# Performance work log

Measured on AMD Instinct MI355X. Metric: run time of the kernel, lower is better.

## Reference

```python
import jax, jax.numpy as jnp
import numpy as np

N = 100000   # nodes
E = 1200000  # edges
D = 64       # in_channels == out_channels, heads=1
NEG_SLOPE = 0.2  # PyG GATv2Conv default negative_slope


def setup_inputs() -> dict:
    key = jax.random.key(0)
    k1, k2, k3, k4 = jax.random.split(key, 4)
    x = jax.random.normal(k1, (N, D), dtype=jnp.float32)
    edge_index = jax.random.randint(k2, (2, E), 0, N, dtype=jnp.int32)
    # glorot-ish scale for shared linear (share_weights=True -> lin_l == lin_r)
    W = jax.random.normal(k3, (D, D), dtype=jnp.float32) * (1.0 / np.sqrt(D))
    b = jnp.zeros((D,), dtype=jnp.float32)
    att = jax.random.normal(k4, (D,), dtype=jnp.float32) * (1.0 / np.sqrt(D))
    return {"x": x, "edge_index": edge_index, "W": W, "b": b, "att": att}


def reference(x, edge_index, W, b, att):
    src = edge_index[0]  # source j (messages flow j -> i)
    dst = edge_index[1]  # target i
    # shared linear transform (share_weights=True)
    z = x @ W.T + b                                   # [N, D]
    # GATv2 score: att . leakyrelu(z_j + z_i)
    e = jax.nn.leaky_relu(z[src] + z[dst], NEG_SLOPE) @ att  # [E]
    # segment softmax over incoming edges of each target node
    m = jax.ops.segment_max(e, dst, num_segments=N)   # [N]
    ex = jnp.exp(e - m[dst])                          # [E]
    s = jax.ops.segment_sum(ex, dst, num_segments=N)  # [N]
    alpha = ex / s[dst]                               # [E]
    # SimpleConv(aggr='sum') with edge_weight=alpha on ORIGINAL x
    out = jax.ops.segment_sum(alpha[:, None] * x[src], dst, num_segments=N)  # [N, D]
    return out
```

## Files before the change

kernel.cpp:

```cpp
#include <hip/hip_runtime.h>

#define D 64
#define LOG2E 1.4426950408889634f

#define HEPT_H 32
#define SEPT 32
#define BSH 7
#define BSZ 128

using frag_ab = __attribute__((ext_vector_type(8))) short;
using f32x4   = __attribute__((ext_vector_type(4))) float;

__device__ __forceinline__ unsigned short f2bf(float f) {
    unsigned int bits = __float_as_uint(f);
    return (unsigned short)((bits + 0x7fffu + ((bits >> 16) & 1u)) >> 16);
}

__device__ __forceinline__ frag_ab pack8(float4 a, float4 b) {
    frag_ab f;
    f[0] = (short)f2bf(a.x); f[1] = (short)f2bf(a.y);
    f[2] = (short)f2bf(a.z); f[3] = (short)f2bf(a.w);
    f[4] = (short)f2bf(b.x); f[5] = (short)f2bf(b.y);
    f[6] = (short)f2bf(b.z); f[7] = (short)f2bf(b.w);
    return f;
}

__global__ __launch_bounds__(256) void gemm_z_hist(const float* __restrict__ x,
                                                   const float* __restrict__ W,
                                                   const float* __restrict__ b,
                                                   unsigned int* __restrict__ zxb,
                                                   int n,
                                                   const int* __restrict__ dst,
                                                   int* __restrict__ hist2d,
                                                   int e_cnt, int histBlk,
                                                   int nb, int nblk) {
    __shared__ int cnt[2048];
    int tid = threadIdx.x;

    if ((int)blockIdx.x < histBlk) {
        for (int i = tid; i < nb; i += 256) cnt[i] = 0;
        __syncthreads();
        int base = blockIdx.x * (256 * HEPT_H);
        for (int j = 0; j < HEPT_H; ++j) {
            int e = base + j * 256 + tid;
            if (e < e_cnt) atomicAdd(&cnt[dst[e] >> BSH], 1);
        }
        __syncthreads();
        for (int i = tid; i < nb; i += 256)
            hist2d[(size_t)i * nblk + blockIdx.x] = cnt[i];
        return;
    }

    int row0 = (blockIdx.x - histBlk) * 64;
    int l  = tid & 63;
    int w  = tid >> 6;
    int lr = l & 15;
    int hi = l >> 4;
    int lk = hi * 8;

    int arow = row0 + w * 16 + lr;
    int crow = (arow < n) ? arow : (n - 1);
    const float* xp = x + (size_t)crow * 64;
    frag_ab afr[2];
#pragma unroll
    for (int ks = 0; ks < 2; ++ks) {
        const float* ap = xp + ks * 32 + lk;
        afr[ks] = pack8(*(const float4*)ap, *(const float4*)(ap + 4));
    }

    frag_ab bfr[4][2];
#pragma unroll
    for (int colt = 0; colt < 4; ++colt) {
#pragma unroll
        for (int ks = 0; ks < 2; ++ks) {
            const float* wp = W + (colt * 16 + lr) * 64 + ks * 32 + lk;
            bfr[colt][ks] = pack8(*(const float4*)wp, *(const float4*)(wp + 4));
        }
    }

    f32x4 zero = {0.f, 0.f, 0.f, 0.f};
    f32x4 acc[4] = {zero, zero, zero, zero};
#pragma unroll
    for (int ks = 0; ks < 2; ++ks) {
#pragma unroll
        for (int colt = 0; colt < 4; ++colt) {
            acc[colt] = __builtin_amdgcn_mfma_f32_16x16x32_bf16(
                afr[ks], bfr[colt][ks], acc[colt], 0, 0, 0);
        }
    }

#pragma unroll
    for (int colt = 0; colt < 4; ++colt) {
        int col = colt * 16 + lr;
        float bb = b[col];
#pragma unroll
        for (int r = 0; r < 4; ++r) {
            int row = row0 + w * 16 + hi * 4 + r;
            int rrow = (row < n) ? row : (n - 1);
            float z  = acc[colt][r] + bb;
            float xv = x[(size_t)rrow * 64 + col];
            unsigned int u = (unsigned int)f2bf(z) |
                             ((unsigned int)f2bf(xv) << 16);
            if (row < n)
                zxb[(size_t)row * 64 + col] = u;
        }
    }
}

__global__ __launch_bounds__(256) void scan_part(const int* __restrict__ data,
                                                 int* __restrict__ part, int n) {
    __shared__ int red[256];
    int t = threadIdx.x;
    int i = blockIdx.x * 256 + t;
    red[t] = (i < n) ? data[i] : 0;
    __syncthreads();
    for (int off = 128; off >= 1; off >>= 1) {
        if (t < off) red[t] += red[t + off];
        __syncthreads();
    }
    if (t == 0) part[blockIdx.x] = red[0];
}

__global__ __launch_bounds__(1024) void scan_top(int* __restrict__ part, int B) {
    __shared__ int s[1024];
    int t = threadIdx.x;
    int v = (t < B) ? part[t] : 0;
    s[t] = v;
    __syncthreads();
    for (int off = 1; off < 1024; off <<= 1) {
        int u = (t >= off) ? s[t - off] : 0;
        __syncthreads();
        s[t] += u;
        __syncthreads();
    }
    if (t < B) part[t] = s[t] - v;
}

__global__ __launch_bounds__(256) void scan_final_ip(int* data,
                                                     const int* __restrict__ part, int n) {
    __shared__ int s[256];
    int t = threadIdx.x;
    int i = blockIdx.x * 256 + t;
    int v = (i < n) ? data[i] : 0;
    s[t] = v;
    __syncthreads();
    for (int off = 1; off < 256; off <<= 1) {
        int u = (t >= off) ? s[t - off] : 0;
        __syncthreads();
        s[t] += u;
        __syncthreads();
    }
    int incl = s[t] + part[blockIdx.x];
    if (i < n) data[i] = incl - v;
    if (i == n - 1) data[n] = incl;
}

__global__ __launch_bounds__(256) void msd_scatter(const int* __restrict__ src,
                                                   const int* __restrict__ dst,
                                                   const int* __restrict__ histS,
                                                   unsigned int* __restrict__ packed,
                                                   int e_cnt, int nb, int nblk) {
    __shared__ int cnt[1024];
    int t = threadIdx.x;
    int blk = blockIdx.x;
    for (int i = t; i < nb; i += 256) cnt[i] = histS[(size_t)i * nblk + blk];
    __syncthreads();
    int base = blk * (256 * SEPT);
    for (int j = 0; j < SEPT; ++j) {
        int e = base + j * 256 + t;
        if (e < e_cnt) {
            int d = dst[e];
            int pos = atomicAdd(&cnt[d >> BSH], 1);
            packed[pos] = (unsigned int)src[e] | ((unsigned int)(d & (BSZ - 1)) << 24);
        }
    }
}

__global__ __launch_bounds__(256) void bucket_csr(const unsigned int* __restrict__ packed,
                                                  const int* __restrict__ histS,
                                                  int* __restrict__ rowstart,
                                                  int* __restrict__ srcids,
                                                  int n, int e_cnt, int nb, int nblk) {
    __shared__ int cnt[128];
    __shared__ int sc[128];
    __shared__ int cur[128];
    int t = threadIdx.x;
    int b = blockIdx.x;
    int lo = histS[(size_t)b * nblk];
    int hi = histS[(size_t)(b + 1) * nblk];
    int m = hi - lo;

    if (t < 128) cnt[t] = 0;
    __syncthreads();
    for (int i = t; i < m; i += 256)
        atomicAdd(&cnt[packed[lo + i] >> 24], 1);
    __syncthreads();
    if (t < 128) sc[t] = cnt[t];
    __syncthreads();
    for (int off = 1; off < 128; off <<= 1) {
        int u = (t < 128 && t >= off) ? sc[t - off] : 0;
        __syncthreads();
        if (t < 128) sc[t] += u;
        __syncthreads();
    }
    if (t < 128) {
        int excl = sc[t] - cnt[t];
        cur[t] = lo + excl;
        int node = (b << BSH) + t;
        if (node < n) rowstart[node] = lo + excl;
    }
    if (b == nb - 1 && t == 0) rowstart[n] = e_cnt;
    __syncthreads();
    for (int i = t; i < m; i += 256) {
        unsigned int p = packed[lo + i];
        int pos = atomicAdd(&cur[p >> 24], 1);
        srcids[pos] = (int)(p & 0xFFFFFFu);
    }
}

__global__ __launch_bounds__(256) void gather4b(const int* __restrict__ srcids,
                                                const int* __restrict__ rowstart,
                                                const unsigned int* __restrict__ zxb,
                                                const float* __restrict__ att,
                                                float* __restrict__ out, int n) {
    int lane = threadIdx.x & 63;
    int node = blockIdx.x * 4 + (threadIdx.x >> 6);
    if (node >= n) return;
    int q = lane & 15;
    int h = lane >> 4;
    int rs = rowstart[node], re = rowstart[node + 1];

    const uint4 zdv = *(const uint4*)(zxb + (size_t)node * 64 + 4 * q);
    float zd0 = __uint_as_float(zdv.x << 16);
    float zd1 = __uint_as_float(zdv.y << 16);
    float zd2 = __uint_as_float(zdv.z << 16);
    float zd3 = __uint_as_float(zdv.w << 16);
    float4 av = *(const float4*)(att + 4 * q);
    float a0 = av.x * LOG2E, a1 = av.y * LOG2E, a2 = av.z * LOG2E, a3 = av.w * LOG2E;

    float ax0 = 0.f, ax1 = 0.f, ax2 = 0.f, ax3 = 0.f, ssum = 0.f;
    int efull = rs + ((re - rs) & ~7);
    int e = rs;
    for (; e < efull; e += 8) {
        int s0 = srcids[e + h];
        int s1 = srcids[e + 4 + h];
        const uint4 r0 = *(const uint4*)(zxb + (size_t)s0 * 64 + 4 * q);
        const uint4 r1 = *(const uint4*)(zxb + (size_t)s1 * 64 + 4 * q);

        float v0 = __uint_as_float(r0.x << 16) + zd0; v0 = fmaxf(v0, 0.2f * v0);
        float v1 = __uint_as_float(r0.y << 16) + zd1; v1 = fmaxf(v1, 0.2f * v1);
        float v2 = __uint_as_float(r0.z << 16) + zd2; v2 = fmaxf(v2, 0.2f * v2);
        float v3 = __uint_as_float(r0.w << 16) + zd3; v3 = fmaxf(v3, 0.2f * v3);
        float p0 = v0 * a0 + v1 * a1 + v2 * a2 + v3 * a3;

        float u0 = __uint_as_float(r1.x << 16) + zd0; u0 = fmaxf(u0, 0.2f * u0);
        float u1 = __uint_as_float(r1.y << 16) + zd1; u1 = fmaxf(u1, 0.2f * u1);
        float u2 = __uint_as_float(r1.z << 16) + zd2; u2 = fmaxf(u2, 0.2f * u2);
        float u3 = __uint_as_float(r1.w << 16) + zd3; u3 = fmaxf(u3, 0.2f * u3);
        float p1 = u0 * a0 + u1 * a1 + u2 * a2 + u3 * a3;

#pragma unroll
        for (int off = 8; off >= 1; off >>= 1) {
            p0 += __shfl_xor(p0, off, 64);
            p1 += __shfl_xor(p1, off, 64);
        }
        float ex0 = __builtin_exp2f(p0);
        float ex1 = __builtin_exp2f(p1);
        ssum += ex0 + ex1;
        ax0 += ex0 * __uint_as_float(r0.x & 0xffff0000u)
             + ex1 * __uint_as_float(r1.x & 0xffff0000u);
        ax1 += ex0 * __uint_as_float(r0.y & 0xffff0000u)
             + ex1 * __uint_as_float(r1.y & 0xffff0000u);
        ax2 += ex0 * __uint_as_float(r0.z & 0xffff0000u)
             + ex1 * __uint_as_float(r1.z & 0xffff0000u);
        ax3 += ex0 * __uint_as_float(r0.w & 0xffff0000u)
             + ex1 * __uint_as_float(r1.w & 0xffff0000u);
    }
    if (e < re) {
        int e0i = e + h, e1i = e + 4 + h;
        bool l0 = e0i < re, l1 = e1i < re;
        int s0 = l0 ? srcids[e0i] : node;
        int s1 = l1 ? srcids[e1i] : node;
        const uint4 r0 = *(const uint4*)(zxb + (size_t)s0 * 64 + 4 * q);
        const uint4 r1 = *(const uint4*)(zxb + (size_t)s1 * 64 + 4 * q);

        float v0 = __uint_as_float(r0.x << 16) + zd0; v0 = fmaxf(v0, 0.2f * v0);
        float v1 = __uint_as_float(r0.y << 16) + zd1; v1 = fmaxf(v1, 0.2f * v1);
        float v2 = __uint_as_float(r0.z << 16) + zd2; v2 = fmaxf(v2, 0.2f * v2);
        float v3 = __uint_as_float(r0.w << 16) + zd3; v3 = fmaxf(v3, 0.2f * v3);
        float p0 = v0 * a0 + v1 * a1 + v2 * a2 + v3 * a3;

        float u0 = __uint_as_float(r1.x << 16) + zd0; u0 = fmaxf(u0, 0.2f * u0);
        float u1 = __uint_as_float(r1.y << 16) + zd1; u1 = fmaxf(u1, 0.2f * u1);
        float u2 = __uint_as_float(r1.z << 16) + zd2; u2 = fmaxf(u2, 0.2f * u2);
        float u3 = __uint_as_float(r1.w << 16) + zd3; u3 = fmaxf(u3, 0.2f * u3);
        float p1 = u0 * a0 + u1 * a1 + u2 * a2 + u3 * a3;

#pragma unroll
        for (int off = 8; off >= 1; off >>= 1) {
            p0 += __shfl_xor(p0, off, 64);
            p1 += __shfl_xor(p1, off, 64);
        }
        float ex0 = l0 ? __builtin_exp2f(p0) : 0.f;
        float ex1 = l1 ? __builtin_exp2f(p1) : 0.f;
        ssum += ex0 + ex1;
        ax0 += ex0 * __uint_as_float(r0.x & 0xffff0000u)
             + ex1 * __uint_as_float(r1.x & 0xffff0000u);
        ax1 += ex0 * __uint_as_float(r0.y & 0xffff0000u)
             + ex1 * __uint_as_float(r1.y & 0xffff0000u);
        ax2 += ex0 * __uint_as_float(r0.z & 0xffff0000u)
             + ex1 * __uint_as_float(r1.z & 0xffff0000u);
        ax3 += ex0 * __uint_as_float(r0.w & 0xffff0000u)
             + ex1 * __uint_as_float(r1.w & 0xffff0000u);
    }
    ssum += __shfl_xor(ssum, 16, 64); ssum += __shfl_xor(ssum, 32, 64);
    ax0  += __shfl_xor(ax0, 16, 64);  ax0  += __shfl_xor(ax0, 32, 64);
    ax1  += __shfl_xor(ax1, 16, 64);  ax1  += __shfl_xor(ax1, 32, 64);
    ax2  += __shfl_xor(ax2, 16, 64);  ax2  += __shfl_xor(ax2, 32, 64);
    ax3  += __shfl_xor(ax3, 16, 64);  ax3  += __shfl_xor(ax3, 32, 64);
    if (h == 0) {
        float inv = (re > rs) ? 1.f / ssum : 0.f;
        float4 o = make_float4(ax0 * inv, ax1 * inv, ax2 * inv, ax3 * inv);
        *(float4*)&out[(size_t)node * D + 4 * q] = o;
    }
}

extern "C" void kernel_launch(void* const* d_in, const int* in_sizes, int n_in,
                              void* d_out, int out_size, void* d_ws, size_t ws_size,
                              hipStream_t stream) {
    const float* x   = (const float*)d_in[0];
    const int*   ei  = (const int*)d_in[1];
    const float* W   = (const float*)d_in[2];
    const float* b   = (const float*)d_in[3];
    const float* att = (const float*)d_in[4];
    int n = in_sizes[0] / D;
    int e = in_sizes[1] / 2;
    const int* src = ei;
    const int* dst = ei + e;
    float* out = (float*)d_out;

    int gemmBlk = (n + 63) / 64;
    int nb      = (n + BSZ - 1) >> BSH;
    int histBlk = (e + 256 * HEPT_H - 1) / (256 * HEPT_H);
    int nblk    = histBlk;
    int scatBlk = (e + 256 * SEPT - 1) / (256 * SEPT);
    int NBH     = nb * nblk;
    int scanBlk = (NBH + 255) / 256;

    unsigned int* zxb = (unsigned int*)d_ws;
    int* hist2d   = (int*)(zxb + (size_t)n * 64);
    int* rowstart = hist2d + NBH + 1;
    int* srcids   = rowstart + n + 1;
    unsigned int* packed = (unsigned int*)(srcids + e);
    int* part     = (int*)(packed + e);

    gemm_z_hist<<<histBlk + gemmBlk, 256, 0, stream>>>(x, W, b, zxb, n,
                                                       dst, hist2d, e, histBlk, nb, nblk);
    scan_part<<<scanBlk, 256, 0, stream>>>(hist2d, part, NBH);
    scan_top<<<1, 1024, 0, stream>>>(part, scanBlk);
    scan_final_ip<<<scanBlk, 256, 0, stream>>>(hist2d, part, NBH);
    msd_scatter<<<scatBlk, 256, 0, stream>>>(src, dst, hist2d, packed, e, nb, nblk);
    bucket_csr<<<nb, 256, 0, stream>>>(packed, hist2d, rowstart, srcids, n, e, nb, nblk);
    gather4b<<<(n + 3) / 4, 256, 0, stream>>>(srcids, rowstart, zxb, att, out, n);
}
```

Baseline: 194.1 us.

## Fuse CSR construction into a single cooperative kernel with grid syncs

Replaces the histogram, three-pass scan, scatter and bucket-CSR kernels with one cooperative kernel that uses grid.sync between phases, with one block per destination bucket (782 blocks). The histogram is split out of the GEMM kernel into its own stage. The aim is to remove several kernel launches and the inter-kernel gaps. In exchange, all blocks must be co-resident, each block processes more edges (~1535) with less parallelism, and the GEMM no longer overlaps with the histogram.

Result: slower. 561.2 us (+189.1%).

```diff
diff --git a/kernel.cpp b/kernel.cpp
--- a/kernel.cpp
+++ b/kernel.cpp
@@ -1,10 +1,11 @@
 #include <hip/hip_runtime.h>
+#include <hip/hip_cooperative_groups.h>
+
+namespace cg = cooperative_groups;
 
 #define D 64
 #define LOG2E 1.4426950408889634f
 
-#define HEPT_H 32
-#define SEPT 32
 #define BSH 7
 #define BSZ 128
 
@@ -25,33 +26,13 @@
     return f;
 }
 
-__global__ __launch_bounds__(256) void gemm_z_hist(const float* __restrict__ x,
-                                                   const float* __restrict__ W,
-                                                   const float* __restrict__ b,
-                                                   unsigned int* __restrict__ zxb,
-                                                   int n,
-                                                   const int* __restrict__ dst,
-                                                   int* __restrict__ hist2d,
-                                                   int e_cnt, int histBlk,
-                                                   int nb, int nblk) {
-    __shared__ int cnt[2048];
+__global__ __launch_bounds__(256) void gemm_z(const float* __restrict__ x,
+                                              const float* __restrict__ W,
+                                              const float* __restrict__ b,
+                                              unsigned int* __restrict__ zxb,
+                                              int n) {
     int tid = threadIdx.x;
-
-    if ((int)blockIdx.x < histBlk) {
-        for (int i = tid; i < nb; i += 256) cnt[i] = 0;
-        __syncthreads();
-        int base = blockIdx.x * (256 * HEPT_H);
-        for (int j = 0; j < HEPT_H; ++j) {
-            int e = base + j * 256 + tid;
-            if (e < e_cnt) atomicAdd(&cnt[dst[e] >> BSH], 1);
-        }
-        __syncthreads();
-        for (int i = tid; i < nb; i += 256)
-            hist2d[(size_t)i * nblk + blockIdx.x] = cnt[i];
-        return;
-    }
-
-    int row0 = (blockIdx.x - histBlk) * 64;
+    int row0 = blockIdx.x * 64;
     int l  = tid & 63;
     int w  = tid >> 6;
     int lr = l & 15;
@@ -107,114 +88,124 @@
     }
 }
 
-__global__ __launch_bounds__(256) void scan_part(const int* __restrict__ data,
-                                                 int* __restrict__ part, int n) {
+__global__ __launch_bounds__(256) void build_csr(const int* __restrict__ src,
+                                                 const int* __restrict__ dst,
+                                                 int* __restrict__ hist2d,
+                                                 int* __restrict__ rowTot,
+                                                 int* __restrict__ rowBase,
+                                                 int* __restrict__ rowstart,
+                                                 int* __restrict__ srcids,
+                                                 unsigned int* __restrict__ packed,
+                                                 int n, int e_cnt, int nb, int G,
+                                                 int EPB) {
+    cg::grid_group grid = cg::this_grid();
+    __shared__ int cnt[1024];
     __shared__ int red[256];
-    int t = threadIdx.x;
-    int i = blockIdx.x * 256 + t;
-    red[t] = (i < n) ? data[i] : 0;
-    __syncthreads();
-    for (int off = 128; off >= 1; off >>= 1) {
-        if (t < off) red[t] += red[t + off];
-        __syncthreads();
-    }
-    if (t == 0) part[blockIdx.x] = red[0];
-}
-
-__global__ __launch_bounds__(1024) void scan_top(int* __restrict__ part, int B) {
-    __shared__ int s[1024];
-    int t = threadIdx.x;
-    int v = (t < B) ? part[t] : 0;
-    s[t] = v;
-    __syncthreads();
-    for (int off = 1; off < 1024; off <<= 1) {
-        int u = (t >= off) ? s[t - off] : 0;
-        __syncthreads();
-        s[t] += u;
-        __syncthreads();
-    }
-    if (t < B) part[t] = s[t] - v;
-}
-
-__global__ __launch_bounds__(256) void scan_final_ip(int* data,
-                                                     const int* __restrict__ part, int n) {
-    __shared__ int s[256];
-    int t = threadIdx.x;
-    int i = blockIdx.x * 256 + t;
-    int v = (i < n) ? data[i] : 0;
-    s[t] = v;
-    __syncthreads();
-    for (int off = 1; off < 256; off <<= 1) {
-        int u = (t >= off) ? s[t - off] : 0;
-        __syncthreads();
-        s[t] += u;
-        __syncthreads();
-    }
-    int incl = s[t] + part[blockIdx.x];
-    if (i < n) data[i] = incl - v;
-    if (i == n - 1) data[n] = incl;
-}
-
-__global__ __launch_bounds__(256) void msd_scatter(const int* __restrict__ src,
-                                                   const int* __restrict__ dst,
-                                                   const int* __restrict__ histS,
-                                                   unsigned int* __restrict__ packed,
-                                                   int e_cnt, int nb, int nblk) {
-    __shared__ int cnt[1024];
-    int t = threadIdx.x;
-    int blk = blockIdx.x;
-    for (int i = t; i < nb; i += 256) cnt[i] = histS[(size_t)i * nblk + blk];
-    __syncthreads();
-    int base = blk * (256 * SEPT);
-    for (int j = 0; j < SEPT; ++j) {
-        int e = base + j * 256 + t;
-        if (e < e_cnt) {
-            int d = dst[e];
-            int pos = atomicAdd(&cnt[d >> BSH], 1);
-            packed[pos] = (unsigned int)src[e] | ((unsigned int)(d & (BSZ - 1)) << 24);
-        }
-    }
-}
-
-__global__ __launch_bounds__(256) void bucket_csr(const unsigned int* __restrict__ packed,
-                                                  const int* __restrict__ histS,
-                                                  int* __restrict__ rowstart,
-                                                  int* __restrict__ srcids,
-                                                  int n, int e_cnt, int nb, int nblk) {
-    __shared__ int cnt[128];
-    __shared__ int sc[128];
     __shared__ int cur[128];
     int t = threadIdx.x;
     int b = blockIdx.x;
-    int lo = histS[(size_t)b * nblk];
-    int hi = histS[(size_t)(b + 1) * nblk];
-    int m = hi - lo;
-
-    if (t < 128) cnt[t] = 0;
+    int elo = b * EPB;
+    int ehi = elo + EPB; if (ehi > e_cnt) ehi = e_cnt;
+
+    for (int i = t; i < nb; i += 256) cnt[i] = 0;
     __syncthreads();
-    for (int i = t; i < m; i += 256)
-        atomicAdd(&cnt[packed[lo + i] >> 24], 1);
+    for (int e = elo + t; e < ehi; e += 256)
+        atomicAdd(&cnt[dst[e] >> BSH], 1);
     __syncthreads();
-    if (t < 128) sc[t] = cnt[t];
+    for (int i = t; i < nb; i += 256)
+        hist2d[(size_t)i * G + b] = cnt[i];
+    grid.sync();
+
+    {
+        int base = b * G;
+        int j0 = 4 * t;
+        int v0 = (j0 + 0 < G) ? hist2d[base + j0 + 0] : 0;
+        int v1 = (j0 + 1 < G) ? hist2d[base + j0 + 1] : 0;
+        int v2 = (j0 + 2 < G) ? hist2d[base + j0 + 2] : 0;
+        int v3 = (j0 + 3 < G) ? hist2d[base + j0 + 3] : 0;
+        int tsum = v0 + v1 + v2 + v3;
+        red[t] = tsum;
+        __syncthreads();
+        for (int off = 1; off < 256; off <<= 1) {
+            int u = (t >= off) ? red[t - off] : 0;
+            __syncthreads();
+            red[t] += u;
+            __syncthreads();
+        }
+        int excl = red[t] - tsum;
+        if (j0 + 0 < G) hist2d[base + j0 + 0] = excl;
+        if (j0 + 1 < G) hist2d[base + j0 + 1] = excl + v0;
+        if (j0 + 2 < G) hist2d[base + j0 + 2] = excl + v0 + v1;
+        if (j0 + 3 < G) hist2d[base + j0 + 3] = excl + v0 + v1 + v2;
+        if (t == 255) rowTot[b] = red[255];
+    }
+    grid.sync();
+
+    if (b == 0) {
+        int j0 = 4 * t;
+        int v0 = (j0 + 0 < nb) ? rowTot[j0 + 0] : 0;
+        int v1 = (j0 + 1 < nb) ? rowTot[j0 + 1] : 0;
+        int v2 = (j0 + 2 < nb) ? rowTot[j0 + 2] : 0;
+        int v3 = (j0 + 3 < nb) ? rowTot[j0 + 3] : 0;
+        int tsum = v0 + v1 + v2 + v3;
+        red[t] = tsum;
+        __syncthreads();
+        for (int off = 1; off < 256; off <<= 1) {
+            int u = (t >= off) ? red[t - off] : 0;
+            __syncthreads();
+            red[t] += u;
+            __syncthreads();
+        }
+        int excl = red[t] - tsum;
+        if (j0 + 0 < nb) rowBase[j0 + 0] = excl;
+        if (j0 + 1 < nb) rowBase[j0 + 1] = excl + v0;
+        if (j0 + 2 < nb) rowBase[j0 + 2] = excl + v0 + v1;
+        if (j0 + 3 < nb) rowBase[j0 + 3] = excl + v0 + v1 + v2;
+        if (t == 255) rowBase[nb] = red[255];
+    }
+    grid.sync();
+
+    for (int i = t; i < nb; i += 256)
+        cnt[i] = rowBase[i] + hist2d[(size_t)i * G + b];
     __syncthreads();
-    for (int off = 1; off < 128; off <<= 1) {
-        int u = (t < 128 && t >= off) ? sc[t - off] : 0;
-        __syncthreads();
-        if (t < 128) sc[t] += u;
-        __syncthreads();
-    }
-    if (t < 128) {
-        int excl = sc[t] - cnt[t];
-        cur[t] = lo + excl;
-        int node = (b << BSH) + t;
-        if (node < n) rowstart[node] = lo + excl;
-    }
-    if (b == nb - 1 && t == 0) rowstart[n] = e_cnt;
-    __syncthreads();
-    for (int i = t; i < m; i += 256) {
-        unsigned int p = packed[lo + i];
-        int pos = atomicAdd(&cur[p >> 24], 1);
-        srcids[pos] = (int)(p & 0xFFFFFFu);
+    for (int e = elo + t; e < ehi; e += 256) {
+        int d = dst[e];
+        int pos = atomicAdd(&cnt[d >> BSH], 1);
+        packed[pos] = (unsigned int)src[e] | ((unsigned int)(d & (BSZ - 1)) << 24);
+    }
+    grid.sync();
+
+    {
+        int lo = rowBase[b];
+        int hi = rowBase[b + 1];
+        int m = hi - lo;
+        if (t < 128) cnt[t] = 0;
+        __syncthreads();
+        for (int i = t; i < m; i += 256)
+            atomicAdd(&cnt[packed[lo + i] >> 24], 1);
+        __syncthreads();
+        int c = (t < 128) ? cnt[t] : 0;
+        red[t] = c;
+        __syncthreads();
+        for (int off = 1; off < 128; off <<= 1) {
+            int u = (t < 128 && t >= off) ? red[t - off] : 0;
+            __syncthreads();
+            if (t < 128) red[t] += u;
+            __syncthreads();
+        }
+        if (t < 128) {
+            int excl = red[t] - c;
+            cur[t] = lo + excl;
+            int node = (b << BSH) + t;
+            if (node < n) rowstart[node] = lo + excl;
+        }
+        if (b == nb - 1 && t == 0) rowstart[n] = e_cnt;
+        __syncthreads();
+        for (int i = t; i < m; i += 256) {
+            unsigned int p = packed[lo + i];
+            int pos = atomicAdd(&cur[p >> 24], 1);
+            srcids[pos] = (int)(p & 0xFFFFFFu);
+        }
     }
 }
 
@@ -341,25 +332,25 @@
 
     int gemmBlk = (n + 63) / 64;
     int nb      = (n + BSZ - 1) >> BSH;
-    int histBlk = (e + 256 * HEPT_H - 1) / (256 * HEPT_H);
-    int nblk    = histBlk;
-    int scatBlk = (e + 256 * SEPT - 1) / (256 * SEPT);
-    int NBH     = nb * nblk;
-    int scanBlk = (NBH + 255) / 256;
+    int G       = nb;
+    int EPB     = (e + G - 1) / G;
 
     unsigned int* zxb = (unsigned int*)d_ws;
     int* hist2d   = (int*)(zxb + (size_t)n * 64);
-    int* rowstart = hist2d + NBH + 1;
+    int* rowTot   = hist2d + (size_t)nb * G;
+    int* rowBase  = rowTot + nb;
+    int* rowstart = rowBase + nb + 1;
     int* srcids   = rowstart + n + 1;
     unsigned int* packed = (unsigned int*)(srcids + e);
-    int* part     = (int*)(packed + e);
-
-    gemm_z_hist<<<histBlk + gemmBlk, 256, 0, stream>>>(x, W, b, zxb, n,
-                                                       dst, hist2d, e, histBlk, nb, nblk);
-    scan_part<<<scanBlk, 256, 0, stream>>>(hist2d, part, NBH);
-    scan_top<<<1, 1024, 0, stream>>>(part, scanBlk);
-    scan_final_ip<<<scanBlk, 256, 0, stream>>>(hist2d, part, NBH);
-    msd_scatter<<<scatBlk, 256, 0, stream>>>(src, dst, hist2d, packed, e, nb, nblk);
-    bucket_csr<<<nb, 256, 0, stream>>>(packed, hist2d, rowstart, srcids, n, e, nb, nblk);
+
+    gemm_z<<<gemmBlk, 256, 0, stream>>>(x, W, b, zxb, n);
+
+    void* args[] = { (void*)&src, (void*)&dst, (void*)&hist2d, (void*)&rowTot,
+                     (void*)&rowBase, (void*)&rowstart, (void*)&srcids,
+                     (void*)&packed, (void*)&n, (void*)&e, (void*)&nb,
+                     (void*)&G, (void*)&EPB };
+    hipLaunchCooperativeKernel((const void*)build_csr, dim3(G), dim3(256),
+                               args, 0, stream);
+
     gather4b<<<(n + 3) / 4, 256, 0, stream>>>(srcids, rowstart, zxb, att, out, n);
 }
```

## Widen counting-sort buckets to 512 nodes and fuse three-pass scan into one kernel

Applied to the files above, without the earlier changes.

Bucket size for the two-level counting sort grows from 128 to 512 nodes, which cuts the bucket count from about 782 to 196 and shrinks the 2D histogram fourfold. The packed word now stores a 17-bit source id and a 9-bit local destination. With the smaller histogram, the three scan kernels are replaced by one 1024-thread block that scans serial per-thread chunks, removing two launches. bucket_csr uses 512 threads per larger bucket, so there is more shared-atomic contention per block and fewer blocks overall. The 17-bit source field only holds ids below 131072, so correctness now depends on N staying under that limit.

New measurement: 235.6 us. 1.21x slower.

```diff
diff --git a/kernel.cpp b/kernel.cpp
--- a/kernel.cpp
+++ b/kernel.cpp
@@ -5,8 +5,8 @@
 
 #define HEPT_H 32
 #define SEPT 32
-#define BSH 7
-#define BSZ 128
+#define BSH 9
+#define BSZ 512
 
 using frag_ab = __attribute__((ext_vector_type(8))) short;
 using f32x4   = __attribute__((ext_vector_type(4))) float;
@@ -34,7 +34,7 @@
                                                    int* __restrict__ hist2d,
                                                    int e_cnt, int histBlk,
                                                    int nb, int nblk) {
-    __shared__ int cnt[2048];
+    __shared__ int cnt[512];
     int tid = threadIdx.x;
 
     if ((int)blockIdx.x < histBlk) {
@@ -107,52 +107,33 @@
     }
 }
 
-__global__ __launch_bounds__(256) void scan_part(const int* __restrict__ data,
-                                                 int* __restrict__ part, int n) {
-    __shared__ int red[256];
+__global__ __launch_bounds__(1024) void scan_all(int* data, int total_n, int C) {
+    __shared__ int tot[1024];
     int t = threadIdx.x;
-    int i = blockIdx.x * 256 + t;
-    red[t] = (i < n) ? data[i] : 0;
-    __syncthreads();
-    for (int off = 128; off >= 1; off >>= 1) {
-        if (t < off) red[t] += red[t + off];
-        __syncthreads();
-    }
-    if (t == 0) part[blockIdx.x] = red[0];
-}
-
-__global__ __launch_bounds__(1024) void scan_top(int* __restrict__ part, int B) {
-    __shared__ int s[1024];
-    int t = threadIdx.x;
-    int v = (t < B) ? part[t] : 0;
-    s[t] = v;
+    int base = t * C;
+    int s = 0;
+    for (int j = 0; j < C; ++j) {
+        int idx = base + j;
+        if (idx < total_n) s += data[idx];
+    }
+    tot[t] = s;
     __syncthreads();
     for (int off = 1; off < 1024; off <<= 1) {
-        int u = (t >= off) ? s[t - off] : 0;
-        __syncthreads();
-        s[t] += u;
-        __syncthreads();
-    }
-    if (t < B) part[t] = s[t] - v;
-}
-
-__global__ __launch_bounds__(256) void scan_final_ip(int* data,
-                                                     const int* __restrict__ part, int n) {
-    __shared__ int s[256];
-    int t = threadIdx.x;
-    int i = blockIdx.x * 256 + t;
-    int v = (i < n) ? data[i] : 0;
-    s[t] = v;
-    __syncthreads();
-    for (int off = 1; off < 256; off <<= 1) {
-        int u = (t >= off) ? s[t - off] : 0;
-        __syncthreads();
-        s[t] += u;
-        __syncthreads();
-    }
-    int incl = s[t] + part[blockIdx.x];
-    if (i < n) data[i] = incl - v;
-    if (i == n - 1) data[n] = incl;
+        int u = (t >= off) ? tot[t - off] : 0;
+        __syncthreads();
+        tot[t] += u;
+        __syncthreads();
+    }
+    int run = tot[t] - s;
+    for (int j = 0; j < C; ++j) {
+        int idx = base + j;
+        if (idx < total_n) {
+            int v = data[idx];
+            data[idx] = run;
+            run += v;
+        }
+    }
+    if (t == 1023) data[total_n] = tot[1023];
 }
 
 __global__ __launch_bounds__(256) void msd_scatter(const int* __restrict__ src,
@@ -160,7 +141,7 @@
                                                    const int* __restrict__ histS,
                                                    unsigned int* __restrict__ packed,
                                                    int e_cnt, int nb, int nblk) {
-    __shared__ int cnt[1024];
+    __shared__ int cnt[512];
     int t = threadIdx.x;
     int blk = blockIdx.x;
     for (int i = t; i < nb; i += 256) cnt[i] = histS[(size_t)i * nblk + blk];
@@ -171,50 +152,50 @@
         if (e < e_cnt) {
             int d = dst[e];
             int pos = atomicAdd(&cnt[d >> BSH], 1);
-            packed[pos] = (unsigned int)src[e] | ((unsigned int)(d & (BSZ - 1)) << 24);
-        }
-    }
-}
-
-__global__ __launch_bounds__(256) void bucket_csr(const unsigned int* __restrict__ packed,
+            packed[pos] = (unsigned int)src[e] |
+                          ((unsigned int)(d & (BSZ - 1)) << 17);
+        }
+    }
+}
+
+__global__ __launch_bounds__(512) void bucket_csr(const unsigned int* __restrict__ packed,
                                                   const int* __restrict__ histS,
                                                   int* __restrict__ rowstart,
                                                   int* __restrict__ srcids,
                                                   int n, int e_cnt, int nb, int nblk) {
-    __shared__ int cnt[128];
-    __shared__ int sc[128];
-    __shared__ int cur[128];
+    __shared__ int cnt[512];
+    __shared__ int red[512];
+    __shared__ int cur[512];
     int t = threadIdx.x;
     int b = blockIdx.x;
     int lo = histS[(size_t)b * nblk];
     int hi = histS[(size_t)(b + 1) * nblk];
     int m = hi - lo;
 
-    if (t < 128) cnt[t] = 0;
-    __syncthreads();
-    for (int i = t; i < m; i += 256)
-        atomicAdd(&cnt[packed[lo + i] >> 24], 1);
-    __syncthreads();
-    if (t < 128) sc[t] = cnt[t];
-    __syncthreads();
-    for (int off = 1; off < 128; off <<= 1) {
-        int u = (t < 128 && t >= off) ? sc[t - off] : 0;
-        __syncthreads();
-        if (t < 128) sc[t] += u;
-        __syncthreads();
-    }
-    if (t < 128) {
-        int excl = sc[t] - cnt[t];
-        cur[t] = lo + excl;
-        int node = (b << BSH) + t;
-        if (node < n) rowstart[node] = lo + excl;
-    }
+    cnt[t] = 0;
+    __syncthreads();
+    for (int i = t; i < m; i += 512)
+        atomicAdd(&cnt[packed[lo + i] >> 17], 1);
+    __syncthreads();
+    int c = cnt[t];
+    red[t] = c;
+    __syncthreads();
+    for (int off = 1; off < 512; off <<= 1) {
+        int u = (t >= off) ? red[t - off] : 0;
+        __syncthreads();
+        red[t] += u;
+        __syncthreads();
+    }
+    int excl = red[t] - c;
+    cur[t] = lo + excl;
+    int node = (b << BSH) + t;
+    if (node < n) rowstart[node] = lo + excl;
     if (b == nb - 1 && t == 0) rowstart[n] = e_cnt;
     __syncthreads();
-    for (int i = t; i < m; i += 256) {
+    for (int i = t; i < m; i += 512) {
         unsigned int p = packed[lo + i];
-        int pos = atomicAdd(&cur[p >> 24], 1);
-        srcids[pos] = (int)(p & 0xFFFFFFu);
+        int pos = atomicAdd(&cur[p >> 17], 1);
+        srcids[pos] = (int)(p & 0x1FFFFu);
     }
 }
 
@@ -345,21 +326,18 @@
     int nblk    = histBlk;
     int scatBlk = (e + 256 * SEPT - 1) / (256 * SEPT);
     int NBH     = nb * nblk;
-    int scanBlk = (NBH + 255) / 256;
+    int chunk   = (NBH + 1023) / 1024;
 
     unsigned int* zxb = (unsigned int*)d_ws;
     int* hist2d   = (int*)(zxb + (size_t)n * 64);
     int* rowstart = hist2d + NBH + 1;
     int* srcids   = rowstart + n + 1;
     unsigned int* packed = (unsigned int*)(srcids + e);
-    int* part     = (int*)(packed + e);
 
     gemm_z_hist<<<histBlk + gemmBlk, 256, 0, stream>>>(x, W, b, zxb, n,
                                                        dst, hist2d, e, histBlk, nb, nblk);
-    scan_part<<<scanBlk, 256, 0, stream>>>(hist2d, part, NBH);
-    scan_top<<<1, 1024, 0, stream>>>(part, scanBlk);
-    scan_final_ip<<<scanBlk, 256, 0, stream>>>(hist2d, part, NBH);
+    scan_all<<<1, 1024, 0, stream>>>(hist2d, NBH, chunk);
     msd_scatter<<<scatBlk, 256, 0, stream>>>(src, dst, hist2d, packed, e, nb, nblk);
-    bucket_csr<<<nb, 256, 0, stream>>>(packed, hist2d, rowstart, srcids, n, e, nb, nblk);
+    bucket_csr<<<nb, 512, 0, stream>>>(packed, hist2d, rowstart, srcids, n, e, nb, nblk);
     gather4b<<<(n + 3) / 4, 256, 0, stream>>>(srcids, rowstart, zxb, att, out, n);
 }
```

## Fuse bucket CSR build into gather kernel and merge scan passes

Applied to the files above, without the earlier changes.

The bucket-to-CSR kernel and the attention gather kernel become one kernel. Each block sorts its 64-node bucket's source ids into shared memory, up to a capacity of 1536, and then processes those nodes directly. If a bucket holds more edges than that, the ids spill to a global fallback buffer. Bucket size drops from 128 to 64 nodes, and the top-level scan kernel is removed by having each final-scan block reduce the partial sums that precede it. This cuts kernel launches and the global round trip for rowstart and srcids, but each block now handles 16 nodes per wave serially with fewer blocks, which can lower parallelism and add load imbalance.

After: 195.9 us. Within noise of the previous version (+0.9%).

```diff
diff --git a/kernel.cpp b/kernel.cpp
--- a/kernel.cpp
+++ b/kernel.cpp
@@ -5,8 +5,9 @@
 
 #define HEPT_H 32
 #define SEPT 32
-#define BSH 7
-#define BSZ 128
+#define BSH 6
+#define BSZ 64
+#define CAP 1536
 
 using frag_ab = __attribute__((ext_vector_type(8))) short;
 using f32x4   = __attribute__((ext_vector_type(4))) float;
@@ -121,26 +122,25 @@
     if (t == 0) part[blockIdx.x] = red[0];
 }
 
-__global__ __launch_bounds__(1024) void scan_top(int* __restrict__ part, int B) {
-    __shared__ int s[1024];
-    int t = threadIdx.x;
-    int v = (t < B) ? part[t] : 0;
-    s[t] = v;
-    __syncthreads();
-    for (int off = 1; off < 1024; off <<= 1) {
-        int u = (t >= off) ? s[t - off] : 0;
-        __syncthreads();
-        s[t] += u;
-        __syncthreads();
-    }
-    if (t < B) part[t] = s[t] - v;
-}
-
-__global__ __launch_bounds__(256) void scan_final_ip(int* data,
-                                                     const int* __restrict__ part, int n) {
+__global__ __launch_bounds__(256) void scan_final2(int* data,
+                                                   const int* __restrict__ part,
+                                                   int n) {
+    __shared__ int red[256];
     __shared__ int s[256];
     int t = threadIdx.x;
-    int i = blockIdx.x * 256 + t;
+    int b = blockIdx.x;
+    int acc = 0;
+    for (int i = t; i < b; i += 256) acc += part[i];
+    red[t] = acc;
+    __syncthreads();
+    for (int off = 128; off >= 1; off >>= 1) {
+        if (t < off) red[t] += red[t + off];
+        __syncthreads();
+    }
+    int base = red[0];
+    __syncthreads();
+
+    int i = b * 256 + t;
     int v = (i < n) ? data[i] : 0;
     s[t] = v;
     __syncthreads();
@@ -150,7 +150,7 @@
         s[t] += u;
         __syncthreads();
     }
-    int incl = s[t] + part[blockIdx.x];
+    int incl = s[t] + base;
     if (i < n) data[i] = incl - v;
     if (i == n - 1) data[n] = incl;
 }
@@ -160,7 +160,7 @@
                                                    const int* __restrict__ histS,
                                                    unsigned int* __restrict__ packed,
                                                    int e_cnt, int nb, int nblk) {
-    __shared__ int cnt[1024];
+    __shared__ int cnt[2048];
     int t = threadIdx.x;
     int blk = blockIdx.x;
     for (int i = t; i < nb; i += 256) cnt[i] = histS[(size_t)i * nblk + blk];
@@ -176,152 +176,157 @@
     }
 }
 
-__global__ __launch_bounds__(256) void bucket_csr(const unsigned int* __restrict__ packed,
+__global__ __launch_bounds__(256) void gather_csr(const unsigned int* __restrict__ packed,
                                                   const int* __restrict__ histS,
-                                                  int* __restrict__ rowstart,
-                                                  int* __restrict__ srcids,
-                                                  int n, int e_cnt, int nb, int nblk) {
-    __shared__ int cnt[128];
-    __shared__ int sc[128];
-    __shared__ int cur[128];
+                                                  int* __restrict__ srcfb,
+                                                  const unsigned int* __restrict__ zxb,
+                                                  const float* __restrict__ att,
+                                                  float* __restrict__ out,
+                                                  int n, int nblk) {
+    __shared__ int srcs[CAP];
+    __shared__ int cnt[BSZ];
+    __shared__ int cur[BSZ];
+    __shared__ int rowst[BSZ + 1];
     int t = threadIdx.x;
-    int b = blockIdx.x;
-    int lo = histS[(size_t)b * nblk];
-    int hi = histS[(size_t)(b + 1) * nblk];
-    int m = hi - lo;
-
-    if (t < 128) cnt[t] = 0;
+    int bkt = blockIdx.x;
+    int lo = histS[(size_t)bkt * nblk];
+    int m  = histS[(size_t)(bkt + 1) * nblk] - lo;
+    bool ovf = (m > CAP);
+
+    if (t < BSZ) cnt[t] = 0;
     __syncthreads();
     for (int i = t; i < m; i += 256)
         atomicAdd(&cnt[packed[lo + i] >> 24], 1);
     __syncthreads();
-    if (t < 128) sc[t] = cnt[t];
-    __syncthreads();
-    for (int off = 1; off < 128; off <<= 1) {
-        int u = (t < 128 && t >= off) ? sc[t - off] : 0;
-        __syncthreads();
-        if (t < 128) sc[t] += u;
-        __syncthreads();
-    }
-    if (t < 128) {
-        int excl = sc[t] - cnt[t];
-        cur[t] = lo + excl;
-        int node = (b << BSH) + t;
-        if (node < n) rowstart[node] = lo + excl;
-    }
-    if (b == nb - 1 && t == 0) rowstart[n] = e_cnt;
+    if (t < BSZ) cur[t] = cnt[t];
+    __syncthreads();
+    for (int off = 1; off < BSZ; off <<= 1) {
+        int u = (t < BSZ && t >= off) ? cur[t - off] : 0;
+        __syncthreads();
+        if (t < BSZ) cur[t] += u;
+        __syncthreads();
+    }
+    if (t < BSZ) {
+        rowst[t] = cur[t] - cnt[t];
+        cur[t]   = cur[t] - cnt[t];
+    }
+    if (t == 0) rowst[BSZ] = m;
     __syncthreads();
     for (int i = t; i < m; i += 256) {
         unsigned int p = packed[lo + i];
         int pos = atomicAdd(&cur[p >> 24], 1);
-        srcids[pos] = (int)(p & 0xFFFFFFu);
-    }
-}
-
-__global__ __launch_bounds__(256) void gather4b(const int* __restrict__ srcids,
-                                                const int* __restrict__ rowstart,
-                                                const unsigned int* __restrict__ zxb,
-                                                const float* __restrict__ att,
-                                                float* __restrict__ out, int n) {
-    int lane = threadIdx.x & 63;
-    int node = blockIdx.x * 4 + (threadIdx.x >> 6);
-    if (node >= n) return;
+        int sv = (int)(p & 0xFFFFFFu);
+        if (!ovf) srcs[pos] = sv;
+        else      srcfb[lo + pos] = sv;
+    }
+    __syncthreads();
+
+    int lane = t & 63;
+    int w    = t >> 6;
     int q = lane & 15;
     int h = lane >> 4;
-    int rs = rowstart[node], re = rowstart[node + 1];
-
-    const uint4 zdv = *(const uint4*)(zxb + (size_t)node * 64 + 4 * q);
-    float zd0 = __uint_as_float(zdv.x << 16);
-    float zd1 = __uint_as_float(zdv.y << 16);
-    float zd2 = __uint_as_float(zdv.z << 16);
-    float zd3 = __uint_as_float(zdv.w << 16);
     float4 av = *(const float4*)(att + 4 * q);
     float a0 = av.x * LOG2E, a1 = av.y * LOG2E, a2 = av.z * LOG2E, a3 = av.w * LOG2E;
-
-    float ax0 = 0.f, ax1 = 0.f, ax2 = 0.f, ax3 = 0.f, ssum = 0.f;
-    int efull = rs + ((re - rs) & ~7);
-    int e = rs;
-    for (; e < efull; e += 8) {
-        int s0 = srcids[e + h];
-        int s1 = srcids[e + 4 + h];
-        const uint4 r0 = *(const uint4*)(zxb + (size_t)s0 * 64 + 4 * q);
-        const uint4 r1 = *(const uint4*)(zxb + (size_t)s1 * 64 + 4 * q);
-
-        float v0 = __uint_as_float(r0.x << 16) + zd0; v0 = fmaxf(v0, 0.2f * v0);
-        float v1 = __uint_as_float(r0.y << 16) + zd1; v1 = fmaxf(v1, 0.2f * v1);
-        float v2 = __uint_as_float(r0.z << 16) + zd2; v2 = fmaxf(v2, 0.2f * v2);
-        float v3 = __uint_as_float(r0.w << 16) + zd3; v3 = fmaxf(v3, 0.2f * v3);
-        float p0 = v0 * a0 + v1 * a1 + v2 * a2 + v3 * a3;
-
-        float u0 = __uint_as_float(r1.x << 16) + zd0; u0 = fmaxf(u0, 0.2f * u0);
-        float u1 = __uint_as_float(r1.y << 16) + zd1; u1 = fmaxf(u1, 0.2f * u1);
-        float u2 = __uint_as_float(r1.z << 16) + zd2; u2 = fmaxf(u2, 0.2f * u2);
-        float u3 = __uint_as_float(r1.w << 16) + zd3; u3 = fmaxf(u3, 0.2f * u3);
-        float p1 = u0 * a0 + u1 * a1 + u2 * a2 + u3 * a3;
-
-#pragma unroll
-        for (int off = 8; off >= 1; off >>= 1) {
-            p0 += __shfl_xor(p0, off, 64);
-            p1 += __shfl_xor(p1, off, 64);
-        }
-        float ex0 = __builtin_exp2f(p0);
-        float ex1 = __builtin_exp2f(p1);
-        ssum += ex0 + ex1;
-        ax0 += ex0 * __uint_as_float(r0.x & 0xffff0000u)
-             + ex1 * __uint_as_float(r1.x & 0xffff0000u);
-        ax1 += ex0 * __uint_as_float(r0.y & 0xffff0000u)
-             + ex1 * __uint_as_float(r1.y & 0xffff0000u);
-        ax2 += ex0 * __uint_as_float(r0.z & 0xffff0000u)
-             + ex1 * __uint_as_float(r1.z & 0xffff0000u);
-        ax3 += ex0 * __uint_as_float(r0.w & 0xffff0000u)
-             + ex1 * __uint_as_float(r1.w & 0xffff0000u);
-    }
-    if (e < re) {
-        int e0i = e + h, e1i = e + 4 + h;
-        bool l0 = e0i < re, l1 = e1i < re;
-        int s0 = l0 ? srcids[e0i] : node;
-        int s1 = l1 ? srcids[e1i] : node;
-        const uint4 r0 = *(const uint4*)(zxb + (size_t)s0 * 64 + 4 * q);
-        const uint4 r1 = *(const uint4*)(zxb + (size_t)s1 * 64 + 4 * q);
-
-        float v0 = __uint_as_float(r0.x << 16) + zd0; v0 = fmaxf(v0, 0.2f * v0);
-        float v1 = __uint_as_float(r0.y << 16) + zd1; v1 = fmaxf(v1, 0.2f * v1);
-        float v2 = __uint_as_float(r0.z << 16) + zd2; v2 = fmaxf(v2, 0.2f * v2);
-        float v3 = __uint_as_float(r0.w << 16) + zd3; v3 = fmaxf(v3, 0.2f * v3);
-        float p0 = v0 * a0 + v1 * a1 + v2 * a2 + v3 * a3;
-
-        float u0 = __uint_as_float(r1.x << 16) + zd0; u0 = fmaxf(u0, 0.2f * u0);
-        float u1 = __uint_as_float(r1.y << 16) + zd1; u1 = fmaxf(u1, 0.2f * u1);
-        float u2 = __uint_as_float(r1.z << 16) + zd2; u2 = fmaxf(u2, 0.2f * u2);
-        float u3 = __uint_as_float(r1.w << 16) + zd3; u3 = fmaxf(u3, 0.2f * u3);
-        float p1 = u0 * a0 + u1 * a1 + u2 * a2 + u3 * a3;
-
-#pragma unroll
-        for (int off = 8; off >= 1; off >>= 1) {
-            p0 += __shfl_xor(p0, off, 64);
-            p1 += __shfl_xor(p1, off, 64);
-        }
-        float ex0 = l0 ? __builtin_exp2f(p0) : 0.f;
-        float ex1 = l1 ? __builtin_exp2f(p1) : 0.f;
-        ssum += ex0 + ex1;
-        ax0 += ex0 * __uint_as_float(r0.x & 0xffff0000u)
-             + ex1 * __uint_as_float(r1.x & 0xffff0000u);
-        ax1 += ex0 * __uint_as_float(r0.y & 0xffff0000u)
-             + ex1 * __uint_as_float(r1.y & 0xffff0000u);
-        ax2 += ex0 * __uint_as_float(r0.z & 0xffff0000u)
-             + ex1 * __uint_as_float(r1.z & 0xffff0000u);
-        ax3 += ex0 * __uint_as_float(r0.w & 0xffff0000u)
-             + ex1 * __uint_as_float(r1.w & 0xffff0000u);
-    }
-    ssum += __shfl_xor(ssum, 16, 64); ssum += __shfl_xor(ssum, 32, 64);
-    ax0  += __shfl_xor(ax0, 16, 64);  ax0  += __shfl_xor(ax0, 32, 64);
-    ax1  += __shfl_xor(ax1, 16, 64);  ax1  += __shfl_xor(ax1, 32, 64);
-    ax2  += __shfl_xor(ax2, 16, 64);  ax2  += __shfl_xor(ax2, 32, 64);
-    ax3  += __shfl_xor(ax3, 16, 64);  ax3  += __shfl_xor(ax3, 32, 64);
-    if (h == 0) {
-        float inv = (re > rs) ? 1.f / ssum : 0.f;
-        float4 o = make_float4(ax0 * inv, ax1 * inv, ax2 * inv, ax3 * inv);
-        *(float4*)&out[(size_t)node * D + 4 * q] = o;
+    const int* sg = srcfb + lo;
+
+    for (int k = 0; k < 16; ++k) {
+        int nl = w * 16 + k;
+        int node = (bkt << BSH) + nl;
+        if (node >= n) break;
+        int rs = rowst[nl], re = rowst[nl + 1];
+
+        const uint4 zdv = *(const uint4*)(zxb + (size_t)node * 64 + 4 * q);
+        float zd0 = __uint_as_float(zdv.x << 16);
+        float zd1 = __uint_as_float(zdv.y << 16);
+        float zd2 = __uint_as_float(zdv.z << 16);
+        float zd3 = __uint_as_float(zdv.w << 16);
+
+        float ax0 = 0.f, ax1 = 0.f, ax2 = 0.f, ax3 = 0.f, ssum = 0.f;
+        int efull = rs + ((re - rs) & ~7);
+        int e = rs;
+        for (; e < efull; e += 8) {
+            int i0 = e + h, i1 = e + 4 + h;
+            int s0 = ovf ? sg[i0] : srcs[i0];
+            int s1 = ovf ? sg[i1] : srcs[i1];
+            const uint4 r0 = *(const uint4*)(zxb + (size_t)s0 * 64 + 4 * q);
+            const uint4 r1 = *(const uint4*)(zxb + (size_t)s1 * 64 + 4 * q);
+
+            float v0 = __uint_as_float(r0.x << 16) + zd0; v0 = fmaxf(v0, 0.2f * v0);
+            float v1 = __uint_as_float(r0.y << 16) + zd1; v1 = fmaxf(v1, 0.2f * v1);
+            float v2 = __uint_as_float(r0.z << 16) + zd2; v2 = fmaxf(v2, 0.2f * v2);
+            float v3 = __uint_as_float(r0.w << 16) + zd3; v3 = fmaxf(v3, 0.2f * v3);
+            float p0 = v0 * a0 + v1 * a1 + v2 * a2 + v3 * a3;
+
+            float u0 = __uint_as_float(r1.x << 16) + zd0; u0 = fmaxf(u0, 0.2f * u0);
+            float u1 = __uint_as_float(r1.y << 16) + zd1; u1 = fmaxf(u1, 0.2f * u1);
+            float u2 = __uint_as_float(r1.z << 16) + zd2; u2 = fmaxf(u2, 0.2f * u2);
+            float u3 = __uint_as_float(r1.w << 16) + zd3; u3 = fmaxf(u3, 0.2f * u3);
+            float p1 = u0 * a0 + u1 * a1 + u2 * a2 + u3 * a3;
+
+#pragma unroll
+            for (int off = 8; off >= 1; off >>= 1) {
+                p0 += __shfl_xor(p0, off, 64);
+                p1 += __shfl_xor(p1, off, 64);
+            }
+            float ex0 = __builtin_exp2f(p0);
+            float ex1 = __builtin_exp2f(p1);
+            ssum += ex0 + ex1;
+            ax0 += ex0 * __uint_as_float(r0.x & 0xffff0000u)
+                 + ex1 * __uint_as_float(r1.x & 0xffff0000u);
+            ax1 += ex0 * __uint_as_float(r0.y & 0xffff0000u)
+                 + ex1 * __uint_as_float(r1.y & 0xffff0000u);
+            ax2 += ex0 * __uint_as_float(r0.z & 0xffff0000u)
+                 + ex1 * __uint_as_float(r1.z & 0xffff0000u);
+            ax3 += ex0 * __uint_as_float(r0.w & 0xffff0000u)
+                 + ex1 * __uint_as_float(r1.w & 0xffff0000u);
+        }
+        if (e < re) {
+            int i0 = e + h, i1 = e + 4 + h;
+            bool l0 = i0 < re, l1 = i1 < re;
+            int s0 = l0 ? (ovf ? sg[i0] : srcs[i0]) : node;
+            int s1 = l1 ? (ovf ? sg[i1] : srcs[i1]) : node;
+            const uint4 r0 = *(const uint4*)(zxb + (size_t)s0 * 64 + 4 * q);
+            const uint4 r1 = *(const uint4*)(zxb + (size_t)s1 * 64 + 4 * q);
+
+            float v0 = __uint_as_float(r0.x << 16) + zd0; v0 = fmaxf(v0, 0.2f * v0);
+            float v1 = __uint_as_float(r0.y << 16) + zd1; v1 = fmaxf(v1, 0.2f * v1);
+            float v2 = __uint_as_float(r0.z << 16) + zd2; v2 = fmaxf(v2, 0.2f * v2);
+            float v3 = __uint_as_float(r0.w << 16) + zd3; v3 = fmaxf(v3, 0.2f * v3);
+            float p0 = v0 * a0 + v1 * a1 + v2 * a2 + v3 * a3;
+
+            float u0 = __uint_as_float(r1.x << 16) + zd0; u0 = fmaxf(u0, 0.2f * u0);
+            float u1 = __uint_as_float(r1.y << 16) + zd1; u1 = fmaxf(u1, 0.2f * u1);
+            float u2 = __uint_as_float(r1.z << 16) + zd2; u2 = fmaxf(u2, 0.2f * u2);
+            float u3 = __uint_as_float(r1.w << 16) + zd3; u3 = fmaxf(u3, 0.2f * u3);
+            float p1 = u0 * a0 + u1 * a1 + u2 * a2 + u3 * a3;
+
+#pragma unroll
+            for (int off = 8; off >= 1; off >>= 1) {
+                p0 += __shfl_xor(p0, off, 64);
+                p1 += __shfl_xor(p1, off, 64);
+            }
+            float ex0 = l0 ? __builtin_exp2f(p0) : 0.f;
+            float ex1 = l1 ? __builtin_exp2f(p1) : 0.f;
+            ssum += ex0 + ex1;
+            ax0 += ex0 * __uint_as_float(r0.x & 0xffff0000u)
+                 + ex1 * __uint_as_float(r1.x & 0xffff0000u);
+            ax1 += ex0 * __uint_as_float(r0.y & 0xffff0000u)
+                 + ex1 * __uint_as_float(r1.y & 0xffff0000u);
+            ax2 += ex0 * __uint_as_float(r0.z & 0xffff0000u)
+                 + ex1 * __uint_as_float(r1.z & 0xffff0000u);
+            ax3 += ex0 * __uint_as_float(r0.w & 0xffff0000u)
+                 + ex1 * __uint_as_float(r1.w & 0xffff0000u);
+        }
+        ssum += __shfl_xor(ssum, 16, 64); ssum += __shfl_xor(ssum, 32, 64);
+        ax0  += __shfl_xor(ax0, 16, 64);  ax0  += __shfl_xor(ax0, 32, 64);
+        ax1  += __shfl_xor(ax1, 16, 64);  ax1  += __shfl_xor(ax1, 32, 64);
+        ax2  += __shfl_xor(ax2, 16, 64);  ax2  += __shfl_xor(ax2, 32, 64);
+        ax3  += __shfl_xor(ax3, 16, 64);  ax3  += __shfl_xor(ax3, 32, 64);
+        if (h == 0) {
+            float inv = (re > rs) ? 1.f / ssum : 0.f;
+            float4 o = make_float4(ax0 * inv, ax1 * inv, ax2 * inv, ax3 * inv);
+            *(float4*)&out[(size_t)node * D + 4 * q] = o;
+        }
     }
 }
 
@@ -349,17 +354,14 @@
 
     unsigned int* zxb = (unsigned int*)d_ws;
     int* hist2d   = (int*)(zxb + (size_t)n * 64);
-    int* rowstart = hist2d + NBH + 1;
-    int* srcids   = rowstart + n + 1;
-    unsigned int* packed = (unsigned int*)(srcids + e);
-    int* part     = (int*)(packed + e);
+    unsigned int* packed = (unsigned int*)(hist2d + NBH + 1);
+    int* srcfb    = (int*)(packed + e);
+    int* part     = srcfb + e;
 
     gemm_z_hist<<<histBlk + gemmBlk, 256, 0, stream>>>(x, W, b, zxb, n,
                                                        dst, hist2d, e, histBlk, nb, nblk);
     scan_part<<<scanBlk, 256, 0, stream>>>(hist2d, part, NBH);
-    scan_top<<<1, 1024, 0, stream>>>(part, scanBlk);
-    scan_final_ip<<<scanBlk, 256, 0, stream>>>(hist2d, part, NBH);
+    scan_final2<<<scanBlk, 256, 0, stream>>>(hist2d, part, NBH);
     msd_scatter<<<scatBlk, 256, 0, stream>>>(src, dst, hist2d, packed, e, nb, nblk);
-    bucket_csr<<<nb, 256, 0, stream>>>(packed, hist2d, rowstart, srcids, n, e, nb, nblk);
-    gather4b<<<(n + 3) / 4, 256, 0, stream>>>(srcids, rowstart, zxb, att, out, n);
-}
+    gather_csr<<<nb, 256, 0, stream>>>(packed, hist2d, srcfb, zxb, att, out, n, nblk);
+}
```
